# Kernel optimization log

Measured on AMD Instinct MI355X. Metric: run time of the kernel, lower is better.

## Reference

```python
import jax, jax.numpy as jnp
import numpy as np

N, K, H, DE, E, TOPK, NHEADS, FFM = 1024, 32, 256, 128, 8, 2, 8, 2


def setup_inputs() -> dict:
    key = jax.random.key(0)
    ks = jax.random.split(key, 20)
    s = 0.02
    node_features = jax.random.normal(ks[0], (N, H), jnp.float32)
    edge_features = jax.random.normal(ks[1], (N, K, H), jnp.float32)
    edge_raw = jax.random.normal(ks[2], (N, K, DE), jnp.float32)
    neighbor_list = jax.random.randint(ks[3], (N, K), 0, N)
    neighbor_mask = (jax.random.uniform(ks[4], (N, K)) < 0.8).astype(jnp.float32)
    # additive attention mask: 0 where key slot is a real neighbor, -1e9 where padded
    attn_mask = jnp.where(neighbor_mask[:, None, :] > 0, 0.0, -1e9).astype(jnp.float32)
    p = lambda k_, shape: jax.random.normal(k_, shape, jnp.float32) * s
    inp = dict(node_features=node_features, edge_features=edge_features,
               edge_raw=edge_raw, neighbor_list=neighbor_list,
               neighbor_mask=neighbor_mask, attn_mask=attn_mask,
               w_gate=p(ks[5], (H, E)),
               W_edge=p(ks[6], (E, DE, H)), b_edge=jnp.zeros((E, H)),
               W_node=p(ks[7], (E, 2 * H, H)), b_node=jnp.zeros((E, H)),
               W_msg=p(ks[8], (E, 2 * H, H)), b_msg=jnp.zeros((E, H)),
               W_qkv=p(ks[9], (E, H, 3 * H)), b_qkv=jnp.zeros((E, 3 * H)),
               W_out=p(ks[10], (E, H, H)), b_out=jnp.zeros((E, H)),
               ln_attn_g=jnp.ones((E, H)), ln_attn_b=jnp.zeros((E, H)),
               ln_ffn_g=jnp.ones((E, H)), ln_ffn_b=jnp.zeros((E, H)),
               W1n=p(ks[11], (E, H, FFM * H)), b1n=jnp.zeros((E, FFM * H)),
               W2n=p(ks[12], (E, FFM * H, H)), b2n=jnp.zeros((E, H)),
               W1e=p(ks[13], (E, H, FFM * H)), b1e=jnp.zeros((E, FFM * H)),
               W2e=p(ks[14], (E, FFM * H, H)), b2e=jnp.zeros((E, H)))
    return inp


def _layernorm(x, g, b):
    mu = x.mean(-1, keepdims=True)
    v = ((x - mu) ** 2).mean(-1, keepdims=True)
    return (x - mu) * jax.lax.rsqrt(v + 1e-5) * g + b


def _moe_forward(node_features, edge_features, edge_raw, neighbor_list,
                 neighbor_mask, attn_mask, w_gate, W_edge, b_edge, W_node,
                 b_node, W_msg, b_msg, W_qkv, b_qkv, W_out, b_out, ln_attn_g,
                 ln_attn_b, ln_ffn_g, ln_ffn_b, W1n, b1n, W2n, b2n, W1e, b1e,
                 W2e, b2e):
    gelu = jax.nn.gelu
    dh = H // NHEADS

    def expert(p):
        (We, be, Wn, bn, Wm, bm, Wqkv, bqkv, Wo, bo,
         lag, lab, lfg, lfb, w1n, c1n, w2n, c2n, w1e, c1e, w2e, c2e) = p
        # --- graph attention sub-block (pre-norm on nodes) ---
        nh = _layernorm(node_features, lag, lab)                 # [N,H]
        eh = gelu(edge_raw @ We + be)                            # [N,K,H]
        sender = nh[neighbor_list]                               # [N,K,H] gather
        recv = jnp.broadcast_to(nh[:, None, :], sender.shape)
        nodeh = gelu(jnp.concatenate([sender, recv], -1) @ Wn + bn)
        msg = gelu(jnp.concatenate([eh, nodeh], -1) @ Wm + bm)   # [N,K,H]
        # multi-head self-attention over each node's neighbor window
        qkv = msg @ Wqkv + bqkv
        q, k_, v = jnp.split(qkv, 3, axis=-1)
        q = q.reshape(N, K, NHEADS, dh)
        k_ = k_.reshape(N, K, NHEADS, dh)
        v = v.reshape(N, K, NHEADS, dh)
        scores = jnp.einsum('nqhd,nkhd->nhqk', q, k_) / np.sqrt(dh).astype(np.float32)
        scores = scores + attn_mask[:, None, :, :]
        attn = jax.nn.softmax(scores, axis=-1)
        edge_out = jnp.einsum('nhqk,nkhd->nqhd', attn, v).reshape(N, K, H) @ Wo + bo
        # masked-mean aggregate of edges -> nodes
        cnt = neighbor_mask.sum(1, keepdims=True) + 1e-5
        node_out = (edge_out * neighbor_mask[..., None]).sum(1) / cnt
        nf = node_out + node_features
        ef = edge_out + edge_features
        # --- feed-forward sub-block ---
        nh2 = _layernorm(nf, lfg, lfb)
        eh2 = _layernorm(ef, lfg, lfb)
        nf = nf + gelu(nh2 @ w1n + c1n) @ w2n + c2n
        ef = ef + gelu(eh2 @ w1e + c1e) @ w2e + c2e
        return nf, ef

    # noisy top-k gating (eval: clean logits, no noise)
    logits = node_features @ w_gate                              # [N,E]
    top_vals, top_idx = jax.lax.top_k(logits, TOPK + 1)
    gk = jax.nn.softmax(top_vals[:, :TOPK], axis=1)
    gates = jnp.zeros_like(logits).at[
        jnp.arange(logits.shape[0])[:, None], top_idx[:, :TOPK]].set(gk)

    stacked = (W_edge, b_edge, W_node, b_node, W_msg, b_msg, W_qkv, b_qkv,
               W_out, b_out, ln_attn_g, ln_attn_b, ln_ffn_g, ln_ffn_b,
               W1n, b1n, W2n, b2n, W1e, b1e, W2e, b2e)
    node_outs, edge_outs = jax.vmap(expert)(stacked)             # [E,N,H],[E,N,K,H]
    node_out = jnp.einsum('ne,enh->nh', gates, node_outs)
    edge_out = jnp.einsum('ne,enkh->nkh', gates, edge_outs)
    return node_out, edge_out


def reference(node_features, edge_features, edge_raw, neighbor_list,
              neighbor_mask, attn_mask, w_gate, W_edge, b_edge, W_node,
              b_node, W_msg, b_msg, W_qkv, b_qkv, W_out, b_out, ln_attn_g,
              ln_attn_b, ln_ffn_g, ln_ffn_b, W1n, b1n, W2n, b2n, W1e, b1e,
              W2e, b2e):
    return _moe_forward(node_features, edge_features, edge_raw, neighbor_list,
                        neighbor_mask, attn_mask, w_gate, W_edge, b_edge,
                        W_node, b_node, W_msg, b_msg, W_qkv, b_qkv, W_out,
                        b_out, ln_attn_g, ln_attn_b, ln_ffn_g, ln_ffn_b,
                        W1n, b1n, W2n, b2n, W1e, b1e, W2e, b2e)
```

## Files before the change

kernel.cpp:

```cpp
#include <hip/hip_runtime.h>
#include <math.h>

#define N_NODES 1024
#define K_NB    32
#define H_DIM   256
#define DE_DIM  128
#define N_EXP   8
#define NTOPK   2
#define FFH     512

typedef __attribute__((ext_vector_type(8))) short s8v;
typedef __attribute__((ext_vector_type(4))) float f4v;

#define NH_ELEMS   (N_EXP * N_NODES * H_DIM)
#define OFF_WN   0
#define OFF_WM   65536
#define OFF_WE   196608
#define OFF_WQ   229376
#define OFF_WO   425984
#define OFF_W1E  491520
#define OFF_W2E  622592
#define EXP_STRIDE 753664

__device__ __forceinline__ unsigned short f2bf(float x) {
  unsigned u = __float_as_uint(x);
  unsigned r = u + 0x7FFFu + ((u >> 16) & 1u);
  return (unsigned short)(r >> 16);
}
__device__ __forceinline__ float bf2f(unsigned short h) {
  return __uint_as_float((unsigned)h << 16);
}
__device__ __forceinline__ float gelu_f(float x) {
  float u = 0.7978845608028654f * (x + 0.044715f * x * x * x);
  float ex = __expf(2.f * u);
  float th = 1.f - 2.f / (ex + 1.f);
  return 0.5f * x * (1.f + th);
}

__device__ __forceinline__ s8v lda(const char* base, int SBv, int rt, int kt, int l) {
  int r = rt * 16 + (l & 15);
  int byte = r * SBv + kt * 64 + ((l >> 4) << 4);
  return *(const s8v*)(base + (byte ^ ((r & 7) << 4)));
}
__device__ __forceinline__ void stb16(char* base, int SBv, int r, int c, float v) {
  *(unsigned short*)(base + ((r * SBv + c * 2) ^ ((r & 7) << 4))) = f2bf(v);
}

template<int NA, int NKT, int CSTR>
__device__ __forceinline__ void kloop2(f4v acc[2][NA], const char* Ab, int ASB,
                                       const unsigned short* __restrict__ fb, int NCT,
                                       int ktb0, int ctb0, int l) {
  __builtin_amdgcn_s_setprio(1);
  for (int kt = 0; kt < NKT; ++kt) {
    s8v a0 = lda(Ab, ASB, 0, kt, l);
    s8v a1 = lda(Ab, ASB, 1, kt, l);
#pragma unroll
    for (int m = 0; m < NA; ++m) {
      s8v bv = *(const s8v*)(fb + (((size_t)(ktb0 + kt) * NCT + (ctb0 + CSTR * m)) * 64 + l) * 8);
      acc[0][m] = __builtin_amdgcn_mfma_f32_16x16x32_bf16(a0, bv, acc[0][m], 0, 0, 0);
      acc[1][m] = __builtin_amdgcn_mfma_f32_16x16x32_bf16(a1, bv, acc[1][m], 0, 0, 0);
    }
  }
  __builtin_amdgcn_s_setprio(0);
}

__global__ __launch_bounds__(64)
void gate_kernel(const float* __restrict__ nf, const float* __restrict__ wg,
                 int* __restrict__ sel_ne, float* __restrict__ sel_g) {
  int n = blockIdx.x, t = threadIdx.x;
  float p[8] = {0, 0, 0, 0, 0, 0, 0, 0};
  for (int j = 0; j < 4; ++j) {
    float x = nf[n * H_DIM + t + 64 * j];
#pragma unroll
    for (int e = 0; e < 8; ++e) p[e] += x * wg[(t + 64 * j) * 8 + e];
  }
#pragma unroll
  for (int e = 0; e < 8; ++e)
    for (int m = 32; m >= 1; m >>= 1) p[e] += __shfl_xor(p[e], m, 64);
  if (t == 0) {
    int i0 = 0; float v0 = p[0];
    for (int e = 1; e < 8; ++e) if (p[e] > v0) { v0 = p[e]; i0 = e; }
    int i1 = -1; float v1 = -3.4e38f;
    for (int e = 0; e < 8; ++e) if (e != i0 && p[e] > v1) { v1 = p[e]; i1 = e; }
    float g1 = __expf(v1 - v0);
    float inv = 1.f / (1.f + g1);
    sel_ne[n * 2 + 0] = (n << 3) | i0; sel_g[n * 2 + 0] = inv;
    sel_ne[n * 2 + 1] = (n << 3) | i1; sel_g[n * 2 + 1] = g1 * inv;
  }
}

__global__ __launch_bounds__(256)
void sort_kernel(const int* __restrict__ sel_ne, const float* __restrict__ sel_g,
                 int* __restrict__ work_ne, float* __restrict__ work_g) {
  __shared__ int cnt[8], off[8], cur[8];
  int t = threadIdx.x;
  if (t < 8) { cnt[t] = 0; cur[t] = 0; }
  __syncthreads();
  for (int i = t; i < N_NODES * NTOPK; i += 256) atomicAdd(&cnt[sel_ne[i] & 7], 1);
  __syncthreads();
  if (t == 0) { int s = 0; for (int e = 0; e < 8; ++e) { off[e] = s; s += cnt[e]; } }
  __syncthreads();
  for (int i = t; i < N_NODES * NTOPK; i += 256) {
    int pe = sel_ne[i]; int e = pe & 7;
    int pos = off[e] + atomicAdd(&cur[e], 1);
    work_ne[pos] = pe; work_g[pos] = sel_g[i];
  }
}

__global__ __launch_bounds__(256)
void nh_kernel(const float* __restrict__ nf, const float* __restrict__ lag,
               const float* __restrict__ lab, unsigned short* __restrict__ nh16) {
  __shared__ float red[8];
  int n = blockIdx.x, e = blockIdx.y, t = threadIdx.x;
  float x = nf[n * H_DIM + t];
  float sv = x, sq = x * x;
  for (int m = 32; m >= 1; m >>= 1) { sv += __shfl_xor(sv, m, 64); sq += __shfl_xor(sq, m, 64); }
  if ((t & 63) == 0) { red[t >> 6] = sv; red[4 + (t >> 6)] = sq; }
  __syncthreads();
  float sum = red[0] + red[1] + red[2] + red[3];
  float ssum = red[4] + red[5] + red[6] + red[7];
  float mu = sum * (1.f / 256.f);
  float var = ssum * (1.f / 256.f) - mu * mu;
  float rstd = rsqrtf(var + 1e-5f);
  nh16[((size_t)e * N_NODES + n) * H_DIM + t] =
      f2bf((x - mu) * rstd * lag[e * H_DIM + t] + lab[e * H_DIM + t]);
}

__global__ __launch_bounds__(64)
void wconv(const float* __restrict__ W_node, const float* __restrict__ W_msg,
           const float* __restrict__ W_edge, const float* __restrict__ W_qkv,
           const float* __restrict__ W_out, const float* __restrict__ W1e,
           const float* __restrict__ W2e, unsigned short* __restrict__ fb) {
  int f = blockIdx.x, e = blockIdx.y, l = threadIdx.x;
  const float* src; int C, nct, fl; size_t off;
  if (f < 128)       { src = W_node + (size_t)e * 131072; C = 256; nct = 16; fl = f;        off = OFF_WN;  }
  else if (f < 384)  { src = W_msg  + (size_t)e * 131072; C = 256; nct = 16; fl = f - 128;  off = OFF_WM;  }
  else if (f < 448)  { src = W_edge + (size_t)e * 32768;  C = 256; nct = 16; fl = f - 384;  off = OFF_WE;  }
  else if (f < 832)  { src = W_qkv  + (size_t)e * 196608; C = 768; nct = 48; fl = f - 448;  off = OFF_WQ;  }
  else if (f < 960)  { src = W_out  + (size_t)e * 65536;  C = 256; nct = 16; fl = f - 832;  off = OFF_WO;  }
  else if (f < 1216) { src = W1e    + (size_t)e * 131072; C = 512; nct = 32; fl = f - 960;  off = OFF_W1E; }
  else               { src = W2e    + (size_t)e * 131072; C = 256; nct = 16; fl = f - 1216; off = OFF_W2E; }
  int kt = fl / nct, ct = fl - kt * nct;
  int k0 = kt * 32 + ((l >> 4) << 3), c = ct * 16 + (l & 15);
  unsigned pk[4];
#pragma unroll
  for (int jj = 0; jj < 4; ++jj) {
    unsigned short a = f2bf(src[(size_t)(k0 + 2 * jj) * C + c]);
    unsigned short b = f2bf(src[(size_t)(k0 + 2 * jj + 1) * C + c]);
    pk[jj] = (unsigned)a | ((unsigned)b << 16);
  }
  unsigned short* dst = fb + (size_t)e * EXP_STRIDE + off + ((size_t)fl * 64 + l) * 8;
  *(uint4*)dst = make_uint4(pk[0], pk[1], pk[2], pk[3]);
}

__global__ __launch_bounds__(512, 4)
void moe_main(const float* __restrict__ node_features,
              const float* __restrict__ edge_features,
              const float* __restrict__ edge_raw,
              const int* __restrict__ neighbor_list,
              const float* __restrict__ neighbor_mask,
              const float* __restrict__ W_node_f32, const float* __restrict__ bn,
              const float* __restrict__ be, const float* __restrict__ bm,
              const float* __restrict__ bq, const float* __restrict__ bo,
              const float* __restrict__ ln_ffn_g, const float* __restrict__ ln_ffn_b,
              const float* __restrict__ W1n, const float* __restrict__ b1n,
              const float* __restrict__ W2n, const float* __restrict__ b2n,
              const float* __restrict__ b1e, const float* __restrict__ b2e,
              const unsigned short* __restrict__ nh16,
              const unsigned short* __restrict__ fb,
              const int* __restrict__ work_ne, const float* __restrict__ work_g,
              float* __restrict__ out_node, float* __restrict__ out_edge) {
  extern __shared__ char sm[];
  char* SAp = sm;
  char* SBp = sm + 16384;
  char* SCp = sm + 32768;
  float* EF = (float*)(sm + 16384);
  char* SDp = sm + 49152;
  char* SQp = sm + 57344;
  float* MF = (float*)(sm + 73728);
  float* Mrecv = MF;
  float* Mrv2  = MF + 256;
  float* Mnp   = MF + 768;
  float* Mnh2  = MF + 1024;
  float* Mh1   = MF + 1280;
  float* Mred  = MF + 1792;
  float* Mmask = MF + 1800;
  float* Mmu   = MF + 1832;
  float* Mrstd = MF + 1864;

  const int t = threadIdx.x;
  const int pe = work_ne[blockIdx.x];
  const int n = pe >> 3, e = pe & 7;
  const float gate = work_g[blockIdx.x];

  const unsigned short* fbE   = fb + (size_t)e * EXP_STRIDE;
  const unsigned short* fbWn  = fbE + OFF_WN;
  const unsigned short* fbWm  = fbE + OFF_WM;
  const unsigned short* fbWe  = fbE + OFF_WE;
  const unsigned short* fbWq  = fbE + OFF_WQ;
  const unsigned short* fbWo  = fbE + OFF_WO;
  const unsigned short* fbW1e = fbE + OFF_W1E;
  const unsigned short* fbW2e = fbE + OFF_W2E;

  const float* Wn2  = W_node_f32 + (size_t)e * 131072;
  const float* bnE  = bn + e * H_DIM;
  const float* beE  = be + e * H_DIM;
  const float* bmE  = bm + e * H_DIM;
  const float* bqE  = bq + e * 3 * H_DIM;
  const float* boE  = bo + e * H_DIM;
  const float* lfg  = ln_ffn_g + e * H_DIM;
  const float* lfb  = ln_ffn_b + e * H_DIM;
  const float* w1n  = W1n + (size_t)e * H_DIM * FFH;
  const float* c1n  = b1n + e * FFH;
  const float* w2n  = W2n + (size_t)e * FFH * H_DIM;
  const float* c2n  = b2n + e * H_DIM;
  const float* c1e  = b1e + e * FFH;
  const float* c2e  = b2e + e * H_DIM;

  const int w = t >> 6, l = t & 63;
  const int ctb = w;
  const int l15 = l & 15, lg = l >> 4;
  const int rbase0 = (lg << 2);

  const unsigned short* nh_e = nh16 + (size_t)e * N_NODES * H_DIM;
#pragma unroll
  for (int rr2 = 0; rr2 < 2; ++rr2) {
    int r = (t >> 5) + 16 * rr2, j = t & 31;
    int nbr = neighbor_list[n * K_NB + r];
    uint4 val = ((const uint4*)(nh_e + (size_t)nbr * H_DIM))[j];
    *(uint4*)(SAp + ((r * 512 + j * 16) ^ ((r & 7) << 4))) = val;
  }
  if (t < 256) Mrecv[t] = bf2f(nh_e[(size_t)n * H_DIM + t]);
#pragma unroll
  for (int rr2 = 0; rr2 < 2; ++rr2) {
    int r = (t >> 5) + 16 * rr2, c = (t & 31) * 4;
    float4 v = *(const float4*)(edge_raw + ((size_t)n * K_NB + r) * DE_DIM + c);
    unsigned p0 = (unsigned)f2bf(v.x) | ((unsigned)f2bf(v.y) << 16);
    unsigned p1 = (unsigned)f2bf(v.z) | ((unsigned)f2bf(v.w) << 16);
    *(uint2*)(SDp + ((r * 256 + c * 2) ^ ((r & 7) << 4))) = make_uint2(p0, p1);
  }
  if (t < 32) Mmask[t] = neighbor_mask[n * K_NB + t];
  if (t < 256) Mnp[t] = 0.f;
  __syncthreads();

  {
    int c = t & 255, part = t >> 8;
    float s0 = 0.f, s1 = 0.f;
    for (int i = 0; i < 64; ++i) {
      s0 += Mrecv[part * 128 + i] * Wn2[(size_t)(256 + part * 128 + i) * 256 + c];
      s1 += Mrecv[part * 128 + 64 + i] * Wn2[(size_t)(256 + part * 128 + 64 + i) * 256 + c];
    }
    Mrv2[part * 256 + c] = s0 + s1;
  }
  __syncthreads();
  if (t < 256) Mrecv[t] = Mrv2[t] + Mrv2[256 + t] + bnE[t];
  __syncthreads();

  {
    f4v acc[2][2];
#pragma unroll
    for (int m = 0; m < 2; ++m) {
      float iv = Mrecv[(ctb + 8 * m) * 16 + l15];
#pragma unroll
      for (int rt2 = 0; rt2 < 2; ++rt2) {
        acc[rt2][m][0] = iv; acc[rt2][m][1] = iv; acc[rt2][m][2] = iv; acc[rt2][m][3] = iv;
      }
    }
    kloop2<2, 8, 8>(acc, SAp, 512, fbWn, 16, 0, ctb, l);
#pragma unroll
    for (int m = 0; m < 2; ++m) {
      int c = (ctb + 8 * m) * 16 + l15;
#pragma unroll
      for (int rt2 = 0; rt2 < 2; ++rt2)
#pragma unroll
        for (int ri = 0; ri < 4; ++ri)
          stb16(SBp, 512, rt2 * 16 + rbase0 + ri, c, gelu_f(acc[rt2][m][ri]));
    }
  }
  {
    f4v acc[2][2];
#pragma unroll
    for (int m = 0; m < 2; ++m) {
      float iv = beE[(ctb + 8 * m) * 16 + l15];
#pragma unroll
      for (int rt2 = 0; rt2 < 2; ++rt2) {
        acc[rt2][m][0] = iv; acc[rt2][m][1] = iv; acc[rt2][m][2] = iv; acc[rt2][m][3] = iv;
      }
    }
    kloop2<2, 4, 8>(acc, SDp, 256, fbWe, 16, 0, ctb, l);
#pragma unroll
    for (int m = 0; m < 2; ++m) {
      int c = (ctb + 8 * m) * 16 + l15;
#pragma unroll
      for (int rt2 = 0; rt2 < 2; ++rt2)
#pragma unroll
        for (int ri = 0; ri < 4; ++ri)
          stb16(SCp, 512, rt2 * 16 + rbase0 + ri, c, gelu_f(acc[rt2][m][ri]));
    }
  }
  __syncthreads();

  {
    f4v acc[2][2];
#pragma unroll
    for (int m = 0; m < 2; ++m) {
      float iv = bmE[(ctb + 8 * m) * 16 + l15];
#pragma unroll
      for (int rt2 = 0; rt2 < 2; ++rt2) {
        acc[rt2][m][0] = iv; acc[rt2][m][1] = iv; acc[rt2][m][2] = iv; acc[rt2][m][3] = iv;
      }
    }
    kloop2<2, 8, 8>(acc, SCp, 512, fbWm, 16, 0, ctb, l);
    kloop2<2, 8, 8>(acc, SBp, 512, fbWm, 16, 8, ctb, l);
#pragma unroll
    for (int m = 0; m < 2; ++m) {
      int c = (ctb + 8 * m) * 16 + l15;
#pragma unroll
      for (int rt2 = 0; rt2 < 2; ++rt2)
#pragma unroll
        for (int ri = 0; ri < 4; ++ri)
          stb16(SAp, 512, rt2 * 16 + rbase0 + ri, c, gelu_f(acc[rt2][m][ri]));
    }
  }
  __syncthreads();

#pragma unroll
  for (int p = 0; p < 3; ++p) {
    f4v acc[2][2];
#pragma unroll
    for (int m = 0; m < 2; ++m) {
      float iv = bqE[(p * 16 + ctb + 8 * m) * 16 + l15];
#pragma unroll
      for (int rt2 = 0; rt2 < 2; ++rt2) {
        acc[rt2][m][0] = iv; acc[rt2][m][1] = iv; acc[rt2][m][2] = iv; acc[rt2][m][3] = iv;
      }
    }
    kloop2<2, 8, 8>(acc, SAp, 512, fbWq, 48, 0, p * 16 + ctb, l);
#pragma unroll
    for (int m = 0; m < 2; ++m) {
      int cg = (p * 16 + ctb + 8 * m) * 16 + l15;
      char* dst = (cg < 256) ? SQp : ((cg < 512) ? SBp : SCp);
      int cl = cg & 255;
#pragma unroll
      for (int rt2 = 0; rt2 < 2; ++rt2)
#pragma unroll
        for (int ri = 0; ri < 4; ++ri)
          stb16(dst, 512, rt2 * 16 + rbase0 + ri, cl, acc[rt2][m][ri]);
    }
  }
  __syncthreads();

  {
    const int h = w;
    f4v st[2][2];
    {
      s8v ka0 = lda(SBp, 512, 0, h, l);
      s8v ka1 = lda(SBp, 512, 1, h, l);
      s8v qb0 = lda(SQp, 512, 0, h, l);
      s8v qb1 = lda(SQp, 512, 1, h, l);
      f4v z = {0.f, 0.f, 0.f, 0.f};
      st[0][0] = __builtin_amdgcn_mfma_f32_16x16x32_bf16(ka0, qb0, z, 0, 0, 0);
      st[0][1] = __builtin_amdgcn_mfma_f32_16x16x32_bf16(ka0, qb1, z, 0, 0, 0);
      st[1][0] = __builtin_amdgcn_mfma_f32_16x16x32_bf16(ka1, qb0, z, 0, 0, 0);
      st[1][1] = __builtin_amdgcn_mfma_f32_16x16x32_bf16(ka1, qb1, z, 0, 0, 0);
    }
    const float scale = 0.17677669529663687f;
    float madd[2][4];
#pragma unroll
    for (int rt2 = 0; rt2 < 2; ++rt2)
#pragma unroll
      for (int ri = 0; ri < 4; ++ri)
        madd[rt2][ri] = (Mmask[rt2 * 16 + 4 * lg + ri] > 0.f) ? 0.f : -1e9f;
#pragma unroll
    for (int ct2 = 0; ct2 < 2; ++ct2) {
      float m_ = -3.4e38f;
#pragma unroll
      for (int rt2 = 0; rt2 < 2; ++rt2)
#pragma unroll
        for (int ri = 0; ri < 4; ++ri) {
          float sv = st[rt2][ct2][ri] * scale + madd[rt2][ri];
          st[rt2][ct2][ri] = sv;
          m_ = fmaxf(m_, sv);
        }
      m_ = fmaxf(m_, __shfl_xor(m_, 16, 64));
      m_ = fmaxf(m_, __shfl_xor(m_, 32, 64));
      float s_ = 0.f;
#pragma unroll
      for (int rt2 = 0; rt2 < 2; ++rt2)
#pragma unroll
        for (int ri = 0; ri < 4; ++ri) {
          float ev = __expf(st[rt2][ct2][ri] - m_);
          st[rt2][ct2][ri] = ev;
          s_ += ev;
        }
      s_ += __shfl_xor(s_, 16, 64);
      s_ += __shfl_xor(s_, 32, 64);
      float inv = 1.f / s_;
#pragma unroll
      for (int rt2 = 0; rt2 < 2; ++rt2)
#pragma unroll
        for (int ri = 0; ri < 4; ++ri)
          stb16(SQp, 512, ct2 * 16 + l15, h * 32 + rt2 * 16 + 4 * lg + ri,
                st[rt2][ct2][ri] * inv);
    }
    s8v pa0 = lda(SQp, 512, 0, h, l);
    s8v pa1 = lda(SQp, 512, 1, h, l);
#pragma unroll
    for (int dt = 0; dt < 2; ++dt) {
      s8v vb;
#pragma unroll
      for (int j = 0; j < 8; ++j) {
        int rj = lg * 8 + j;
        vb[j] = *(const short*)(SCp +
                 ((rj * 512 + h * 64 + dt * 32 + l15 * 2) ^ ((rj & 7) << 4)));
      }
      f4v z = {0.f, 0.f, 0.f, 0.f};
      f4v c0 = __builtin_amdgcn_mfma_f32_16x16x32_bf16(pa0, vb, z, 0, 0, 0);
      f4v c1 = __builtin_amdgcn_mfma_f32_16x16x32_bf16(pa1, vb, z, 0, 0, 0);
#pragma unroll
      for (int ri = 0; ri < 4; ++ri) {
        stb16(SAp, 512, 4 * lg + ri,      h * 32 + dt * 16 + l15, c0[ri]);
        stb16(SAp, 512, 16 + 4 * lg + ri, h * 32 + dt * 16 + l15, c1[ri]);
      }
    }
  }
  __syncthreads();

  {
    f4v acc[2][2];
#pragma unroll
    for (int m = 0; m < 2; ++m) {
      float iv = boE[(ctb + 8 * m) * 16 + l15];
#pragma unroll
      for (int rt2 = 0; rt2 < 2; ++rt2) {
        acc[rt2][m][0] = iv; acc[rt2][m][1] = iv; acc[rt2][m][2] = iv; acc[rt2][m][3] = iv;
      }
    }
    kloop2<2, 8, 8>(acc, SAp, 512, fbWo, 16, 0, ctb, l);
#pragma unroll
    for (int m = 0; m < 2; ++m) {
      int c = (ctb + 8 * m) * 16 + l15;
      float np = 0.f;
#pragma unroll
      for (int rt2 = 0; rt2 < 2; ++rt2)
#pragma unroll
        for (int ri = 0; ri < 4; ++ri) {
          int r = rt2 * 16 + rbase0 + ri;
          float eo = acc[rt2][m][ri];
          np += eo * Mmask[r];
          EF[r * 256 + c] = eo + edge_features[((size_t)n * K_NB + r) * H_DIM + c];
        }
      atomicAdd(&Mnp[c], np);
    }
  }
  __syncthreads();

  {
    int rr = t >> 4, j = t & 15;
    float s1 = 0.f, s2 = 0.f;
#pragma unroll
    for (int m2 = 0; m2 < 16; ++m2) {
      float xv = EF[rr * 256 + j + 16 * m2];
      s1 += xv; s2 += xv * xv;
    }
    s1 += __shfl_xor(s1, 8, 64); s2 += __shfl_xor(s2, 8, 64);
    s1 += __shfl_xor(s1, 4, 64); s2 += __shfl_xor(s2, 4, 64);
    s1 += __shfl_xor(s1, 2, 64); s2 += __shfl_xor(s2, 2, 64);
    s1 += __shfl_xor(s1, 1, 64); s2 += __shfl_xor(s2, 1, 64);
    if (j == 0) {
      float mu2 = s1 * (1.f / 256.f);
      float v2 = s2 * (1.f / 256.f) - mu2 * mu2;
      Mmu[rr] = mu2; Mrstd[rr] = rsqrtf(v2 + 1e-5f);
    }
  }
  float cntv = 1e-5f;
#pragma unroll
  for (int kk = 0; kk < 32; ++kk) cntv += Mmask[kk];
  float nfv = 0.f;
  if (t < 256) {
    nfv = Mnp[t] / cntv + node_features[n * H_DIM + t];
    float sv = nfv, sq = nfv * nfv;
    for (int m = 32; m >= 1; m >>= 1) { sv += __shfl_xor(sv, m, 64); sq += __shfl_xor(sq, m, 64); }
    if ((t & 63) == 0) { Mred[t >> 6] = sv; Mred[4 + (t >> 6)] = sq; }
  }
  __syncthreads();

  if (t < 256) {
    float sum = Mred[0] + Mred[1] + Mred[2] + Mred[3];
    float ssum = Mred[4] + Mred[5] + Mred[6] + Mred[7];
    float mu = sum * (1.f / 256.f);
    float var = ssum * (1.f / 256.f) - mu * mu;
    float rstd = rsqrtf(var + 1e-5f);
    Mnh2[t] = (nfv - mu) * rstd * lfg[t] + lfb[t];
  }
  {
    int col = t & 255, rgp = t >> 8;
    float g2 = lfg[col], b2v = lfb[col];
#pragma unroll
    for (int r8 = 0; r8 < 16; ++r8) {
      int row = rgp * 16 + r8;
      float xv = (EF[row * 256 + col] - Mmu[row]) * Mrstd[row] * g2 + b2v;
      stb16(SAp, 512, row, col, xv);
    }
  }
  __syncthreads();

  f4v acc2[2][2];
#pragma unroll
  for (int m = 0; m < 2; ++m) {
    float iv = c2e[(ctb + 8 * m) * 16 + l15];
#pragma unroll
    for (int rt2 = 0; rt2 < 2; ++rt2) {
      acc2[rt2][m][0] = iv; acc2[rt2][m][1] = iv; acc2[rt2][m][2] = iv; acc2[rt2][m][3] = iv;
    }
  }
#pragma unroll
  for (int half = 0; half < 2; ++half) {
    {
      f4v acc[2][2];
#pragma unroll
      for (int m = 0; m < 2; ++m) {
        float iv = c1e[(half * 16 + ctb + 8 * m) * 16 + l15];
#pragma unroll
        for (int rt2 = 0; rt2 < 2; ++rt2) {
          acc[rt2][m][0] = iv; acc[rt2][m][1] = iv; acc[rt2][m][2] = iv; acc[rt2][m][3] = iv;
        }
      }
      kloop2<2, 8, 8>(acc, SAp, 512, fbW1e, 32, 0, half * 16 + ctb, l);
#pragma unroll
      for (int m = 0; m < 2; ++m) {
        int c = (ctb + 8 * m) * 16 + l15;
#pragma unroll
        for (int rt2 = 0; rt2 < 2; ++rt2)
#pragma unroll
          for (int ri = 0; ri < 4; ++ri)
            stb16(SQp, 512, rt2 * 16 + rbase0 + ri, c, gelu_f(acc[rt2][m][ri]));
      }
    }
    if (half == 0) {
      float a0 = 0.f, a1 = 0.f;
      for (int i = 0; i < 128; ++i) {
        a0 += Mnh2[i] * w1n[(size_t)i * FFH + t];
        a1 += Mnh2[128 + i] * w1n[(size_t)(128 + i) * FFH + t];
      }
      Mh1[t] = gelu_f(a0 + a1 + c1n[t]);
    }
    __syncthreads();
    kloop2<2, 8, 8>(acc2, SQp, 512, fbW2e, 16, half * 8, ctb, l);
    __syncthreads();
  }

#pragma unroll
  for (int m = 0; m < 2; ++m) {
    int c = (ctb + 8 * m) * 16 + l15;
#pragma unroll
    for (int rt2 = 0; rt2 < 2; ++rt2)
#pragma unroll
      for (int ri = 0; ri < 4; ++ri) {
        int r = rt2 * 16 + rbase0 + ri;
        float o = acc2[rt2][m][ri] + EF[r * 256 + c];
        atomicAdd(&out_edge[((size_t)n * K_NB + r) * H_DIM + c], gate * o);
      }
  }
  if (t < 256) {
    float o0 = 0.f, o1 = 0.f, o2 = 0.f, o3 = 0.f;
    for (int i = 0; i < 128; ++i) {
      o0 += Mh1[i]       * w2n[(size_t)i * H_DIM + t];
      o1 += Mh1[128 + i] * w2n[(size_t)(128 + i) * H_DIM + t];
      o2 += Mh1[256 + i] * w2n[(size_t)(256 + i) * H_DIM + t];
      o3 += Mh1[384 + i] * w2n[(size_t)(384 + i) * H_DIM + t];
    }
    float o = nfv + c2n[t] + ((o0 + o1) + (o2 + o3));
    atomicAdd(&out_node[n * H_DIM + t], gate * o);
  }
}

extern "C" void kernel_launch(void* const* d_in, const int* in_sizes, int n_in,
                              void* d_out, int out_size, void* d_ws, size_t ws_size,
                              hipStream_t stream) {
  const float* node_features = (const float*)d_in[0];
  const float* edge_features = (const float*)d_in[1];
  const float* edge_raw      = (const float*)d_in[2];
  const int*   neighbor_list = (const int*)d_in[3];
  const float* neighbor_mask = (const float*)d_in[4];
  const float* w_gate        = (const float*)d_in[6];
  const float* W_edge = (const float*)d_in[7];
  const float* b_edge = (const float*)d_in[8];
  const float* W_node = (const float*)d_in[9];
  const float* b_node = (const float*)d_in[10];
  const float* W_msg  = (const float*)d_in[11];
  const float* b_msg  = (const float*)d_in[12];
  const float* W_qkv  = (const float*)d_in[13];
  const float* b_qkv  = (const float*)d_in[14];
  const float* W_out  = (const float*)d_in[15];
  const float* b_out  = (const float*)d_in[16];
  const float* ln_attn_g = (const float*)d_in[17];
  const float* ln_attn_b = (const float*)d_in[18];
  const float* ln_ffn_g  = (const float*)d_in[19];
  const float* ln_ffn_b  = (const float*)d_in[20];
  const float* W1n = (const float*)d_in[21];
  const float* b1n = (const float*)d_in[22];
  const float* W2n = (const float*)d_in[23];
  const float* b2n = (const float*)d_in[24];
  const float* W1e = (const float*)d_in[25];
  const float* b1e = (const float*)d_in[26];
  const float* W2e = (const float*)d_in[27];
  const float* b2e = (const float*)d_in[28];

  unsigned short* nh16 = (unsigned short*)d_ws;
  unsigned short* fbp  = nh16 + NH_ELEMS;
  int*   sel_ne  = (int*)(fbp + (size_t)N_EXP * EXP_STRIDE);
  float* sel_g   = (float*)(sel_ne + 2048);
  int*   work_ne = (int*)(sel_g + 2048);
  float* work_g  = (float*)(work_ne + 2048);

  float* out_node = (float*)d_out;
  float* out_edge = out_node + N_NODES * H_DIM;

  hipMemsetAsync(d_out, 0, (size_t)out_size * sizeof(float), stream);

  gate_kernel<<<N_NODES, 64, 0, stream>>>(node_features, w_gate, sel_ne, sel_g);
  sort_kernel<<<1, 256, 0, stream>>>(sel_ne, sel_g, work_ne, work_g);
  nh_kernel<<<dim3(N_NODES, N_EXP), 256, 0, stream>>>(node_features, ln_attn_g, ln_attn_b, nh16);
  wconv<<<dim3(1472, N_EXP), 64, 0, stream>>>(W_node, W_msg, W_edge, W_qkv, W_out, W1e, W2e, fbp);

  size_t smem = 81408;
  hipFuncSetAttribute((const void*)moe_main, hipFuncAttributeMaxDynamicSharedMemorySize, (int)smem);
  moe_main<<<N_NODES * NTOPK, 512, smem, stream>>>(
      node_features, edge_features, edge_raw, neighbor_list, neighbor_mask,
      W_node, b_node, b_edge, b_msg, b_qkv, b_out,
      ln_ffn_g, ln_ffn_b, W1n, b1n, W2n, b2n, b1e, b2e,
      nh16, fbp, work_ne, work_g, out_node, out_edge);
}
```

Measured before the change: 632.8 us.

## Move node FFN out of main kernel into batched per-expert MFMA kernel

Removes the per-block scalar fp32 node FFN (W1n/W2n matvecs) from moe_main. moe_main now writes the pre-FFN node vectors to workspace, and a new node_ffn kernel batches 16 same-expert rows per block so it can use bf16 MFMA against pre-converted W1n/W2n. The sort kernel builds a padded per-expert index list for this batching, and wconv converts two more weight tensors. The cost is an extra launch, a workspace round trip, a larger weight conversion pass, and bf16 precision on the node FFN path.

```diff
diff --git a/kernel.cpp b/kernel.cpp
--- a/kernel.cpp
+++ b/kernel.cpp
@@ -8,6 +8,9 @@
 #define N_EXP   8
 #define NTOPK   2
 #define FFH     512
+
+#define NP_PAD  2176
+#define NP_BLK  136
 
 typedef __attribute__((ext_vector_type(8))) short s8v;
 typedef __attribute__((ext_vector_type(4))) float f4v;
@@ -20,7 +23,9 @@
 #define OFF_WO   425984
 #define OFF_W1E  491520
 #define OFF_W2E  622592
-#define EXP_STRIDE 753664
+#define OFF_W1N  753664
+#define OFF_W2N  884736
+#define EXP_STRIDE 1015808
 
 __device__ __forceinline__ unsigned short f2bf(float x) {
   unsigned u = __float_as_uint(x);
@@ -91,19 +96,29 @@
 
 __global__ __launch_bounds__(256)
 void sort_kernel(const int* __restrict__ sel_ne, const float* __restrict__ sel_g,
-                 int* __restrict__ work_ne, float* __restrict__ work_g) {
-  __shared__ int cnt[8], off[8], cur[8];
+                 int* __restrict__ work_ne, float* __restrict__ work_g,
+                 int* __restrict__ pwork) {
+  __shared__ int cnt[8], off[8], poff[8], cur[8];
   int t = threadIdx.x;
   if (t < 8) { cnt[t] = 0; cur[t] = 0; }
+  for (int i = t; i < NP_PAD; i += 256) pwork[i] = -1;
   __syncthreads();
   for (int i = t; i < N_NODES * NTOPK; i += 256) atomicAdd(&cnt[sel_ne[i] & 7], 1);
   __syncthreads();
-  if (t == 0) { int s = 0; for (int e = 0; e < 8; ++e) { off[e] = s; s += cnt[e]; } }
+  if (t == 0) {
+    int s = 0, ps = 0;
+    for (int e = 0; e < 8; ++e) {
+      off[e] = s; s += cnt[e];
+      poff[e] = ps; ps += (cnt[e] + 15) & ~15;
+    }
+  }
   __syncthreads();
   for (int i = t; i < N_NODES * NTOPK; i += 256) {
     int pe = sel_ne[i]; int e = pe & 7;
-    int pos = off[e] + atomicAdd(&cur[e], 1);
+    int ci = atomicAdd(&cur[e], 1);
+    int pos = off[e] + ci;
     work_ne[pos] = pe; work_g[pos] = sel_g[i];
+    pwork[poff[e] + ci] = pos;
   }
 }
 
@@ -130,7 +145,8 @@
 void wconv(const float* __restrict__ W_node, const float* __restrict__ W_msg,
            const float* __restrict__ W_edge, const float* __restrict__ W_qkv,
            const float* __restrict__ W_out, const float* __restrict__ W1e,
-           const float* __restrict__ W2e, unsigned short* __restrict__ fb) {
+           const float* __restrict__ W2e, const float* __restrict__ W1n,
+           const float* __restrict__ W2n, unsigned short* __restrict__ fb) {
   int f = blockIdx.x, e = blockIdx.y, l = threadIdx.x;
   const float* src; int C, nct, fl; size_t off;
   if (f < 128)       { src = W_node + (size_t)e * 131072; C = 256; nct = 16; fl = f;        off = OFF_WN;  }
@@ -139,7 +155,9 @@
   else if (f < 832)  { src = W_qkv  + (size_t)e * 196608; C = 768; nct = 48; fl = f - 448;  off = OFF_WQ;  }
   else if (f < 960)  { src = W_out  + (size_t)e * 65536;  C = 256; nct = 16; fl = f - 832;  off = OFF_WO;  }
   else if (f < 1216) { src = W1e    + (size_t)e * 131072; C = 512; nct = 32; fl = f - 960;  off = OFF_W1E; }
-  else               { src = W2e    + (size_t)e * 131072; C = 256; nct = 16; fl = f - 1216; off = OFF_W2E; }
+  else if (f < 1472) { src = W2e    + (size_t)e * 131072; C = 256; nct = 16; fl = f - 1216; off = OFF_W2E; }
+  else if (f < 1728) { src = W1n    + (size_t)e * 131072; C = 512; nct = 32; fl = f - 1472; off = OFF_W1N; }
+  else               { src = W2n    + (size_t)e * 131072; C = 256; nct = 16; fl = f - 1728; off = OFF_W2N; }
   int kt = fl / nct, ct = fl - kt * nct;
   int k0 = kt * 32 + ((l >> 4) << 3), c = ct * 16 + (l & 15);
   unsigned pk[4];
@@ -151,6 +169,119 @@
   }
   unsigned short* dst = fb + (size_t)e * EXP_STRIDE + off + ((size_t)fl * 64 + l) * 8;
   *(uint4*)dst = make_uint4(pk[0], pk[1], pk[2], pk[3]);
+}
+
+__global__ __launch_bounds__(512)
+void node_ffn(const int* __restrict__ work_ne, const float* __restrict__ work_g,
+              const int* __restrict__ pwork, const float* __restrict__ nfv_ws,
+              const unsigned short* __restrict__ fb,
+              const float* __restrict__ b1n, const float* __restrict__ b2n,
+              const float* __restrict__ ln_ffn_g, const float* __restrict__ ln_ffn_b,
+              float* __restrict__ out_node) {
+  __shared__ char LNb[8192];
+  __shared__ char H1b[16384];
+  __shared__ float NF[16 * 256];
+  __shared__ int Sidx[16]; __shared__ float Sg[16]; __shared__ int Sn[16];
+  __shared__ int Se;
+  const int t = threadIdx.x, b = blockIdx.x;
+  if (t < 16) {
+    int idx = pwork[b * 16 + t];
+    Sidx[t] = idx;
+    Sg[t] = (idx >= 0) ? work_g[idx] : 0.f;
+    Sn[t] = (idx >= 0) ? (work_ne[idx] >> 3) : 0;
+  }
+  if (t == 0) {
+    int e = 0;
+    for (int i = 0; i < 16; ++i) {
+      int ix = pwork[b * 16 + i];
+      if (ix >= 0) { e = work_ne[ix] & 7; break; }
+    }
+    Se = e;
+  }
+  __syncthreads();
+  const int e = Se;
+  const unsigned short* fb1 = fb + (size_t)e * EXP_STRIDE + OFF_W1N;
+  const unsigned short* fb2 = fb + (size_t)e * EXP_STRIDE + OFF_W2N;
+  const float* lfg = ln_ffn_g + e * H_DIM;
+  const float* lfb = ln_ffn_b + e * H_DIM;
+  const float* c1n = b1n + e * FFH;
+  const float* c2n = b2n + e * H_DIM;
+  {
+    int r = t >> 5, j = t & 31;
+    int idx = Sidx[r];
+    float x[8]; float s1 = 0.f, s2 = 0.f;
+#pragma unroll
+    for (int z = 0; z < 8; ++z) {
+      int c = j + 32 * z;
+      float v = (idx >= 0) ? nfv_ws[(size_t)idx * 256 + c] : 0.f;
+      NF[r * 256 + c] = v; x[z] = v; s1 += v; s2 += v * v;
+    }
+    s1 += __shfl_xor(s1, 16, 32); s2 += __shfl_xor(s2, 16, 32);
+    s1 += __shfl_xor(s1, 8, 32);  s2 += __shfl_xor(s2, 8, 32);
+    s1 += __shfl_xor(s1, 4, 32);  s2 += __shfl_xor(s2, 4, 32);
+    s1 += __shfl_xor(s1, 2, 32);  s2 += __shfl_xor(s2, 2, 32);
+    s1 += __shfl_xor(s1, 1, 32);  s2 += __shfl_xor(s2, 1, 32);
+    float mu = s1 * (1.f / 256.f);
+    float var = s2 * (1.f / 256.f) - mu * mu;
+    float rstd = rsqrtf(var + 1e-5f);
+#pragma unroll
+    for (int z = 0; z < 8; ++z) {
+      int c = j + 32 * z;
+      stb16(LNb, 512, r, c, (x[z] - mu) * rstd * lfg[c] + lfb[c]);
+    }
+  }
+  __syncthreads();
+  const int w = t >> 6, l = t & 63, l15 = l & 15, lg = l >> 4;
+  {
+    f4v acc[4];
+#pragma unroll
+    for (int m = 0; m < 4; ++m) {
+      float iv = c1n[(w + 8 * m) * 16 + l15];
+      acc[m][0] = iv; acc[m][1] = iv; acc[m][2] = iv; acc[m][3] = iv;
+    }
+    for (int kt = 0; kt < 8; ++kt) {
+      s8v a = lda(LNb, 512, 0, kt, l);
+#pragma unroll
+      for (int m = 0; m < 4; ++m) {
+        s8v bv = *(const s8v*)(fb1 + (((size_t)kt * 32 + (w + 8 * m)) * 64 + l) * 8);
+        acc[m] = __builtin_amdgcn_mfma_f32_16x16x32_bf16(a, bv, acc[m], 0, 0, 0);
+      }
+    }
+#pragma unroll
+    for (int m = 0; m < 4; ++m) {
+      int c = (w + 8 * m) * 16 + l15;
+#pragma unroll
+      for (int ri = 0; ri < 4; ++ri)
+        stb16(H1b, 1024, 4 * lg + ri, c, gelu_f(acc[m][ri]));
+    }
+  }
+  __syncthreads();
+  {
+    f4v acc[2];
+#pragma unroll
+    for (int m = 0; m < 2; ++m) {
+      float iv = c2n[(w + 8 * m) * 16 + l15];
+      acc[m][0] = iv; acc[m][1] = iv; acc[m][2] = iv; acc[m][3] = iv;
+    }
+    for (int kt = 0; kt < 16; ++kt) {
+      s8v a = lda(H1b, 1024, 0, kt, l);
+#pragma unroll
+      for (int m = 0; m < 2; ++m) {
+        s8v bv = *(const s8v*)(fb2 + (((size_t)kt * 16 + (w + 8 * m)) * 64 + l) * 8);
+        acc[m] = __builtin_amdgcn_mfma_f32_16x16x32_bf16(a, bv, acc[m], 0, 0, 0);
+      }
+    }
+#pragma unroll
+    for (int m = 0; m < 2; ++m) {
+      int c = (w + 8 * m) * 16 + l15;
+#pragma unroll
+      for (int ri = 0; ri < 4; ++ri) {
+        int r = 4 * lg + ri;
+        float o = NF[r * 256 + c] + acc[m][ri];
+        atomicAdd(&out_node[(size_t)Sn[r] * H_DIM + c], Sg[r] * o);
+      }
+    }
+  }
 }
 
 __global__ __launch_bounds__(512, 4)
@@ -163,13 +294,11 @@
               const float* __restrict__ be, const float* __restrict__ bm,
               const float* __restrict__ bq, const float* __restrict__ bo,
               const float* __restrict__ ln_ffn_g, const float* __restrict__ ln_ffn_b,
-              const float* __restrict__ W1n, const float* __restrict__ b1n,
-              const float* __restrict__ W2n, const float* __restrict__ b2n,
               const float* __restrict__ b1e, const float* __restrict__ b2e,
               const unsigned short* __restrict__ nh16,
               const unsigned short* __restrict__ fb,
               const int* __restrict__ work_ne, const float* __restrict__ work_g,
-              float* __restrict__ out_node, float* __restrict__ out_edge) {
+              float* __restrict__ nfv_ws, float* __restrict__ out_edge) {
   extern __shared__ char sm[];
   char* SAp = sm;
   char* SBp = sm + 16384;
@@ -181,12 +310,9 @@
   float* Mrecv = MF;
   float* Mrv2  = MF + 256;
   float* Mnp   = MF + 768;
-  float* Mnh2  = MF + 1024;
-  float* Mh1   = MF + 1280;
-  float* Mred  = MF + 1792;
-  float* Mmask = MF + 1800;
-  float* Mmu   = MF + 1832;
-  float* Mrstd = MF + 1864;
+  float* Mmask = MF + 1024;
+  float* Mmu   = MF + 1056;
+  float* Mrstd = MF + 1088;
 
   const int t = threadIdx.x;
   const int pe = work_ne[blockIdx.x];
@@ -210,10 +336,6 @@
   const float* boE  = bo + e * H_DIM;
   const float* lfg  = ln_ffn_g + e * H_DIM;
   const float* lfb  = ln_ffn_b + e * H_DIM;
-  const float* w1n  = W1n + (size_t)e * H_DIM * FFH;
-  const float* c1n  = b1n + e * FFH;
-  const float* w2n  = W2n + (size_t)e * FFH * H_DIM;
-  const float* c2n  = b2n + e * H_DIM;
   const float* c1e  = b1e + e * FFH;
   const float* c2e  = b2e + e * H_DIM;
 
@@ -476,23 +598,12 @@
   float cntv = 1e-5f;
 #pragma unroll
   for (int kk = 0; kk < 32; ++kk) cntv += Mmask[kk];
-  float nfv = 0.f;
   if (t < 256) {
-    nfv = Mnp[t] / cntv + node_features[n * H_DIM + t];
-    float sv = nfv, sq = nfv * nfv;
-    for (int m = 32; m >= 1; m >>= 1) { sv += __shfl_xor(sv, m, 64); sq += __shfl_xor(sq, m, 64); }
-    if ((t & 63) == 0) { Mred[t >> 6] = sv; Mred[4 + (t >> 6)] = sq; }
-  }
-  __syncthreads();
-
-  if (t < 256) {
-    float sum = Mred[0] + Mred[1] + Mred[2] + Mred[3];
-    float ssum = Mred[4] + Mred[5] + Mred[6] + Mred[7];
-    float mu = sum * (1.f / 256.f);
-    float var = ssum * (1.f / 256.f) - mu * mu;
-    float rstd = rsqrtf(var + 1e-5f);
-    Mnh2[t] = (nfv - mu) * rstd * lfg[t] + lfb[t];
-  }
+    float nfv = Mnp[t] / cntv + node_features[n * H_DIM + t];
+    nfv_ws[(size_t)blockIdx.x * H_DIM + t] = nfv;
+  }
+  __syncthreads();
+
   {
     int col = t & 255, rgp = t >> 8;
     float g2 = lfg[col], b2v = lfb[col];
@@ -537,14 +648,6 @@
             stb16(SQp, 512, rt2 * 16 + rbase0 + ri, c, gelu_f(acc[rt2][m][ri]));
       }
     }
-    if (half == 0) {
-      float a0 = 0.f, a1 = 0.f;
-      for (int i = 0; i < 128; ++i) {
-        a0 += Mnh2[i] * w1n[(size_t)i * FFH + t];
-        a1 += Mnh2[128 + i] * w1n[(size_t)(128 + i) * FFH + t];
-      }
-      Mh1[t] = gelu_f(a0 + a1 + c1n[t]);
-    }
     __syncthreads();
     kloop2<2, 8, 8>(acc2, SQp, 512, fbW2e, 16, half * 8, ctb, l);
     __syncthreads();
@@ -561,17 +664,6 @@
         float o = acc2[rt2][m][ri] + EF[r * 256 + c];
         atomicAdd(&out_edge[((size_t)n * K_NB + r) * H_DIM + c], gate * o);
       }
-  }
-  if (t < 256) {
-    float o0 = 0.f, o1 = 0.f, o2 = 0.f, o3 = 0.f;
-    for (int i = 0; i < 128; ++i) {
-      o0 += Mh1[i]       * w2n[(size_t)i * H_DIM + t];
-      o1 += Mh1[128 + i] * w2n[(size_t)(128 + i) * H_DIM + t];
-      o2 += Mh1[256 + i] * w2n[(size_t)(256 + i) * H_DIM + t];
-      o3 += Mh1[384 + i] * w2n[(size_t)(384 + i) * H_DIM + t];
-    }
-    float o = nfv + c2n[t] + ((o0 + o1) + (o2 + o3));
-    atomicAdd(&out_node[n * H_DIM + t], gate * o);
   }
 }
 
@@ -609,10 +701,13 @@
 
   unsigned short* nh16 = (unsigned short*)d_ws;
   unsigned short* fbp  = nh16 + NH_ELEMS;
-  int*   sel_ne  = (int*)(fbp + (size_t)N_EXP * EXP_STRIDE);
+  unsigned short* endfb = fbp + (size_t)N_EXP * EXP_STRIDE;
+  int*   sel_ne  = (int*)endfb;
   float* sel_g   = (float*)(sel_ne + 2048);
   int*   work_ne = (int*)(sel_g + 2048);
   float* work_g  = (float*)(work_ne + 2048);
+  int*   pwork   = (int*)(work_g + 2048);
+  float* nfv_ws  = (float*)(pwork + NP_PAD);
 
   float* out_node = (float*)d_out;
   float* out_edge = out_node + N_NODES * H_DIM;
@@ -620,15 +715,19 @@
   hipMemsetAsync(d_out, 0, (size_t)out_size * sizeof(float), stream);
 
   gate_kernel<<<N_NODES, 64, 0, stream>>>(node_features, w_gate, sel_ne, sel_g);
-  sort_kernel<<<1, 256, 0, stream>>>(sel_ne, sel_g, work_ne, work_g);
+  sort_kernel<<<1, 256, 0, stream>>>(sel_ne, sel_g, work_ne, work_g, pwork);
   nh_kernel<<<dim3(N_NODES, N_EXP), 256, 0, stream>>>(node_features, ln_attn_g, ln_attn_b, nh16);
-  wconv<<<dim3(1472, N_EXP), 64, 0, stream>>>(W_node, W_msg, W_edge, W_qkv, W_out, W1e, W2e, fbp);
+  wconv<<<dim3(1984, N_EXP), 64, 0, stream>>>(W_node, W_msg, W_edge, W_qkv, W_out,
+                                              W1e, W2e, W1n, W2n, fbp);
 
   size_t smem = 81408;
   hipFuncSetAttribute((const void*)moe_main, hipFuncAttributeMaxDynamicSharedMemorySize, (int)smem);
   moe_main<<<N_NODES * NTOPK, 512, smem, stream>>>(
       node_features, edge_features, edge_raw, neighbor_list, neighbor_mask,
       W_node, b_node, b_edge, b_msg, b_qkv, b_out,
-      ln_ffn_g, ln_ffn_b, W1n, b1n, W2n, b2n, b1e, b2e,
-      nh16, fbp, work_ne, work_g, out_node, out_edge);
-}
+      ln_ffn_g, ln_ffn_b, b1e, b2e,
+      nh16, fbp, work_ne, work_g, nfv_ws, out_edge);
+
+  node_ffn<<<NP_BLK, 512, 0, stream>>>(work_ne, work_g, pwork, nfv_ws, fbp,
+                                       b1n, b2n, ln_ffn_g, ln_ffn_b, out_node);
+}
```

After: 512.2 us. 1.24x faster.
